# Performance work log

Hardware: AMD Instinct MI355X
Metric: run time of the kernel (lower is better)

## Reference

```python
import jax, jax.numpy as jnp
import numpy as np

B, N, DIM, HEADS = 2, 2048, 1024, 16
DH = DIM // HEADS
SCALE = DH ** -0.5


def setup_inputs() -> dict:
    key = jax.random.key(0)
    k1, k2, k3, k4 = jax.random.split(key, 4)
    x = jax.random.normal(k1, (B, N, DIM), dtype=jnp.float32)
    # nn.Linear weights stored as [out, in]; apply as x @ W.T
    w_qkv = jax.random.normal(k2, (3 * DIM, DIM), dtype=jnp.float32) * (DIM ** -0.5)
    w_out = jax.random.normal(k3, (DIM, DIM), dtype=jnp.float32) * (DIM ** -0.5)
    b_out = jax.random.normal(k4, (DIM,), dtype=jnp.float32) * 0.01
    return {"x": x, "w_qkv": w_qkv, "w_out": w_out, "b_out": b_out}


def reference(x, w_qkv, w_out, b_out):
    b, n, _ = x.shape
    qkv = jnp.einsum('bnd,ed->bne', x, w_qkv)  # [b, n, 3*dim]
    q, k, v = jnp.split(qkv, 3, axis=-1)
    # [b, n, dim] -> [b, heads, n, dim_head]
    def split_heads(t):
        return t.reshape(b, n, HEADS, DH).transpose(0, 2, 1, 3)
    q, k, v = split_heads(q), split_heads(k), split_heads(v)
    attn = jnp.einsum('bhid,bhjd->bhij', q, k) * SCALE  # [b, h, n, n]
    attn = jax.nn.softmax(attn, axis=-1)
    out = jnp.einsum('bhij,bhjd->bhid', attn, v)  # [b, h, n, dh]
    out = out.transpose(0, 2, 1, 3).reshape(b, n, DIM)
    return jnp.einsum('bnd,ed->bne', out, w_out) + b_out
```

## Files before the change

kernel.cpp:

```cpp
#include <hip/hip_runtime.h>
#include <hip/hip_bf16.h>
#include <stdint.h>

#define BB 2
#define NN 2048
#define DIMM 1024
#define HEADS 16
#define DH 64
#define E3 3072
#define LOG2E_ 1.44269504088896f
#define THR_ 8.0f

typedef __bf16 bf16;
typedef __attribute__((ext_vector_type(8))) __bf16 bf16x8;
typedef __attribute__((ext_vector_type(4))) __bf16 bf16x4;
typedef __attribute__((ext_vector_type(4))) float f32x4;

__device__ __forceinline__ void gload_lds16(const void* gsrc, void* ldst) {
  __builtin_amdgcn_global_load_lds(
      (const __attribute__((address_space(1))) uint32_t*)(uintptr_t)gsrc,
      (__attribute__((address_space(3))) uint32_t*)(uintptr_t)ldst,
      16, 0, 0);
}

__global__ __launch_bounds__(256)
void convert_all(const float* __restrict__ x, const float* __restrict__ wqkv,
                 const float* __restrict__ wout,
                 bf16* __restrict__ xb, bf16* __restrict__ wqb, bf16* __restrict__ wob) {
  size_t i = (size_t)blockIdx.x * blockDim.x + threadIdx.x;
  const float* src;
  bf16* dst;
  size_t off;
  if (i < 1048576u) { src = x; dst = xb; off = i; }
  else if (i < 1048576u + 786432u) { src = wqkv; dst = wqb; off = i - 1048576u; }
  else { src = wout; dst = wob; off = i - (1048576u + 786432u); }
  float4 v = ((const float4*)src)[off];
  bf16x4 o;
  o[0] = (bf16)v.x; o[1] = (bf16)v.y; o[2] = (bf16)v.z; o[3] = (bf16)v.w;
  *(bf16x4*)(dst + off * 4) = o;
}

#define GDSR(dst, base, off) \
  asm volatile("ds_read_b128 %0, %1 offset:%c2" : "=v"(dst) : "v"(base), "i"(off))

#define GRD12(ABASE, BBASE, OFF) \
  GDSR(af0, ABASE, (OFF));        GDSR(af1, ABASE, (OFF)+2048); \
  GDSR(af2, ABASE, (OFF)+4096);   GDSR(af3, ABASE, (OFF)+6144); \
  GDSR(af4, ABASE, (OFF)+8192);   GDSR(af5, ABASE, (OFF)+10240); \
  GDSR(af6, ABASE, (OFF)+12288);  GDSR(af7, ABASE, (OFF)+14336); \
  GDSR(bf0, BBASE, (OFF));        GDSR(bf1, BBASE, (OFF)+2048); \
  GDSR(bf2, BBASE, (OFF)+4096);   GDSR(bf3, BBASE, (OFF)+6144);

#define GMM32() \
  acc[0][0]=__builtin_amdgcn_mfma_f32_16x16x32_bf16(af0,bf0,acc[0][0],0,0,0); \
  acc[0][1]=__builtin_amdgcn_mfma_f32_16x16x32_bf16(af0,bf1,acc[0][1],0,0,0); \
  acc[0][2]=__builtin_amdgcn_mfma_f32_16x16x32_bf16(af0,bf2,acc[0][2],0,0,0); \
  acc[0][3]=__builtin_amdgcn_mfma_f32_16x16x32_bf16(af0,bf3,acc[0][3],0,0,0); \
  acc[1][0]=__builtin_amdgcn_mfma_f32_16x16x32_bf16(af1,bf0,acc[1][0],0,0,0); \
  acc[1][1]=__builtin_amdgcn_mfma_f32_16x16x32_bf16(af1,bf1,acc[1][1],0,0,0); \
  acc[1][2]=__builtin_amdgcn_mfma_f32_16x16x32_bf16(af1,bf2,acc[1][2],0,0,0); \
  acc[1][3]=__builtin_amdgcn_mfma_f32_16x16x32_bf16(af1,bf3,acc[1][3],0,0,0); \
  acc[2][0]=__builtin_amdgcn_mfma_f32_16x16x32_bf16(af2,bf0,acc[2][0],0,0,0); \
  acc[2][1]=__builtin_amdgcn_mfma_f32_16x16x32_bf16(af2,bf1,acc[2][1],0,0,0); \
  acc[2][2]=__builtin_amdgcn_mfma_f32_16x16x32_bf16(af2,bf2,acc[2][2],0,0,0); \
  acc[2][3]=__builtin_amdgcn_mfma_f32_16x16x32_bf16(af2,bf3,acc[2][3],0,0,0); \
  acc[3][0]=__builtin_amdgcn_mfma_f32_16x16x32_bf16(af3,bf0,acc[3][0],0,0,0); \
  acc[3][1]=__builtin_amdgcn_mfma_f32_16x16x32_bf16(af3,bf1,acc[3][1],0,0,0); \
  acc[3][2]=__builtin_amdgcn_mfma_f32_16x16x32_bf16(af3,bf2,acc[3][2],0,0,0); \
  acc[3][3]=__builtin_amdgcn_mfma_f32_16x16x32_bf16(af3,bf3,acc[3][3],0,0,0); \
  acc[4][0]=__builtin_amdgcn_mfma_f32_16x16x32_bf16(af4,bf0,acc[4][0],0,0,0); \
  acc[4][1]=__builtin_amdgcn_mfma_f32_16x16x32_bf16(af4,bf1,acc[4][1],0,0,0); \
  acc[4][2]=__builtin_amdgcn_mfma_f32_16x16x32_bf16(af4,bf2,acc[4][2],0,0,0); \
  acc[4][3]=__builtin_amdgcn_mfma_f32_16x16x32_bf16(af4,bf3,acc[4][3],0,0,0); \
  acc[5][0]=__builtin_amdgcn_mfma_f32_16x16x32_bf16(af5,bf0,acc[5][0],0,0,0); \
  acc[5][1]=__builtin_amdgcn_mfma_f32_16x16x32_bf16(af5,bf1,acc[5][1],0,0,0); \
  acc[5][2]=__builtin_amdgcn_mfma_f32_16x16x32_bf16(af5,bf2,acc[5][2],0,0,0); \
  acc[5][3]=__builtin_amdgcn_mfma_f32_16x16x32_bf16(af5,bf3,acc[5][3],0,0,0); \
  acc[6][0]=__builtin_amdgcn_mfma_f32_16x16x32_bf16(af6,bf0,acc[6][0],0,0,0); \
  acc[6][1]=__builtin_amdgcn_mfma_f32_16x16x32_bf16(af6,bf1,acc[6][1],0,0,0); \
  acc[6][2]=__builtin_amdgcn_mfma_f32_16x16x32_bf16(af6,bf2,acc[6][2],0,0,0); \
  acc[6][3]=__builtin_amdgcn_mfma_f32_16x16x32_bf16(af6,bf3,acc[6][3],0,0,0); \
  acc[7][0]=__builtin_amdgcn_mfma_f32_16x16x32_bf16(af7,bf0,acc[7][0],0,0,0); \
  acc[7][1]=__builtin_amdgcn_mfma_f32_16x16x32_bf16(af7,bf1,acc[7][1],0,0,0); \
  acc[7][2]=__builtin_amdgcn_mfma_f32_16x16x32_bf16(af7,bf2,acc[7][2],0,0,0); \
  acc[7][3]=__builtin_amdgcn_mfma_f32_16x16x32_bf16(af7,bf3,acc[7][3],0,0,0);

#define GSTAGE(BUF) { \
  gload_lds16(pA,          smem + (BUF)*32768 + w*1024); \
  gload_lds16(pA + 65536,  smem + (BUF)*32768 + 8192 + w*1024); \
  gload_lds16(pA + 131072, smem + (BUF)*32768 + 16384 + w*1024); \
  gload_lds16(pA + 196608, smem + (BUF)*32768 + 24576 + w*1024); \
  gload_lds16(pB,          smem + 65536 + (BUF)*32768 + w*1024); \
  gload_lds16(pB + 65536,  smem + 65536 + (BUF)*32768 + 8192 + w*1024); \
  gload_lds16(pB + 131072, smem + 65536 + (BUF)*32768 + 16384 + w*1024); \
  gload_lds16(pB + 196608, smem + 65536 + (BUF)*32768 + 24576 + w*1024); \
  pA += 64; pB += 64; }

#define GSTEP(BUF, DOSTAGE) { \
  bf16x8 af0, af1, af2, af3, af4, af5, af6, af7, bf0, bf1, bf2, bf3; \
  GRD12(abase0, bbase0, (BUF)*32768); \
  if (DOSTAGE) { GSTAGE((BUF)^1); } \
  asm volatile("s_waitcnt lgkmcnt(0)" ::: "memory"); \
  __builtin_amdgcn_sched_barrier(0); \
  __builtin_amdgcn_s_setprio(1); \
  GMM32(); \
  __builtin_amdgcn_s_setprio(0); \
  GRD12(abase1, bbase1, (BUF)*32768); \
  asm volatile("s_waitcnt lgkmcnt(0)" ::: "memory"); \
  __builtin_amdgcn_sched_barrier(0); \
  __builtin_amdgcn_s_setprio(1); \
  GMM32(); \
  __builtin_amdgcn_s_setprio(0); \
  if (DOSTAGE) { asm volatile("s_waitcnt vmcnt(0)" ::: "memory"); } \
  __builtin_amdgcn_sched_barrier(0); \
  __builtin_amdgcn_s_barrier(); \
}

__global__ __launch_bounds__(512, 2)
void gemm_qkv(const bf16* __restrict__ A, const bf16* __restrict__ Bw,
              bf16* __restrict__ C) {
  int bid = blockIdx.x;
  bid = (bid & 7) * 24 + (bid >> 3);
  const int nx = bid % 12;
  const int ny = bid / 12;
  const int m0 = ny * 256, n0 = nx * 256;
  const int tid = threadIdx.x;
  const int w = tid >> 6, lane = tid & 63, c = lane & 15, g = lane >> 4;
  const int wr = w >> 2, wc = w & 3;

  __shared__ __align__(16) char smem[131072];
  const uint32_t smem32 = (uint32_t)(uintptr_t)smem;
  const uint32_t abase0 = smem32 + (wr * 128 + c) * 128 + ((g ^ (c & 7)) * 16);
  const uint32_t abase1 = smem32 + (wr * 128 + c) * 128 + (((4 + g) ^ (c & 7)) * 16);
  const uint32_t bbase0 = smem32 + 65536 + (wc * 64 + c) * 128 + ((g ^ (c & 7)) * 16);
  const uint32_t bbase1 = smem32 + 65536 + (wc * 64 + c) * 128 + (((4 + g) ^ (c & 7)) * 16);

  const bf16 *pA, *pB;
  {
    const int r0 = tid >> 3;
    const int cc = (tid & 7) ^ ((tid >> 3) & 7);
    pA = A + (size_t)(m0 + r0) * 1024 + cc * 8;
    pB = Bw + (size_t)(n0 + r0) * 1024 + cc * 8;
  }

  f32x4 acc[8][4] = {};

  GSTAGE(0);
  asm volatile("s_waitcnt vmcnt(0)" ::: "memory");
  __builtin_amdgcn_sched_barrier(0);
  __builtin_amdgcn_s_barrier();

  for (int u = 0; u < 7; ++u) {
    GSTEP(0, 1) GSTEP(1, 1)
  }
  GSTEP(0, 1)
  GSTEP(1, 0)

  const float qsc = (n0 < 1024) ? 0.125f : 1.0f;
#pragma unroll
  for (int fr = 0; fr < 8; ++fr) {
    const int row = m0 + wr * 128 + fr * 16 + g * 4;
#pragma unroll
    for (int fc = 0; fc < 4; ++fc) {
      const int col = n0 + wc * 64 + fc * 16 + c;
#pragma unroll
      for (int r = 0; r < 4; ++r)
        C[(size_t)(row + r) * E3 + col] = (bf16)(acc[fr][fc][r] * qsc);
    }
  }
}

#define ORD8(ABASE, BBASE, OFF) \
  GDSR(ao0, ABASE, (OFF));        GDSR(ao1, ABASE, (OFF)+2048); \
  GDSR(ao2, ABASE, (OFF)+4096);   GDSR(ao3, ABASE, (OFF)+6144); \
  GDSR(bo0, BBASE, (OFF));        GDSR(bo1, BBASE, (OFF)+2048); \
  GDSR(bo2, BBASE, (OFF)+4096);   GDSR(bo3, BBASE, (OFF)+6144);

#define OMM16() \
  acc[0][0]=__builtin_amdgcn_mfma_f32_16x16x32_bf16(ao0,bo0,acc[0][0],0,0,0); \
  acc[0][1]=__builtin_amdgcn_mfma_f32_16x16x32_bf16(ao0,bo1,acc[0][1],0,0,0); \
  acc[0][2]=__builtin_amdgcn_mfma_f32_16x16x32_bf16(ao0,bo2,acc[0][2],0,0,0); \
  acc[0][3]=__builtin_amdgcn_mfma_f32_16x16x32_bf16(ao0,bo3,acc[0][3],0,0,0); \
  acc[1][0]=__builtin_amdgcn_mfma_f32_16x16x32_bf16(ao1,bo0,acc[1][0],0,0,0); \
  acc[1][1]=__builtin_amdgcn_mfma_f32_16x16x32_bf16(ao1,bo1,acc[1][1],0,0,0); \
  acc[1][2]=__builtin_amdgcn_mfma_f32_16x16x32_bf16(ao1,bo2,acc[1][2],0,0,0); \
  acc[1][3]=__builtin_amdgcn_mfma_f32_16x16x32_bf16(ao1,bo3,acc[1][3],0,0,0); \
  acc[2][0]=__builtin_amdgcn_mfma_f32_16x16x32_bf16(ao2,bo0,acc[2][0],0,0,0); \
  acc[2][1]=__builtin_amdgcn_mfma_f32_16x16x32_bf16(ao2,bo1,acc[2][1],0,0,0); \
  acc[2][2]=__builtin_amdgcn_mfma_f32_16x16x32_bf16(ao2,bo2,acc[2][2],0,0,0); \
  acc[2][3]=__builtin_amdgcn_mfma_f32_16x16x32_bf16(ao2,bo3,acc[2][3],0,0,0); \
  acc[3][0]=__builtin_amdgcn_mfma_f32_16x16x32_bf16(ao3,bo0,acc[3][0],0,0,0); \
  acc[3][1]=__builtin_amdgcn_mfma_f32_16x16x32_bf16(ao3,bo1,acc[3][1],0,0,0); \
  acc[3][2]=__builtin_amdgcn_mfma_f32_16x16x32_bf16(ao3,bo2,acc[3][2],0,0,0); \
  acc[3][3]=__builtin_amdgcn_mfma_f32_16x16x32_bf16(ao3,bo3,acc[3][3],0,0,0);

#define OSTAGE(BUF) { \
  gload_lds16(pA,          smem + (BUF)*16384 + w*1024); \
  gload_lds16(pA + 32768,  smem + (BUF)*16384 + 4096 + w*1024); \
  gload_lds16(pA + 65536,  smem + (BUF)*16384 + 8192 + w*1024); \
  gload_lds16(pA + 98304,  smem + (BUF)*16384 + 12288 + w*1024); \
  gload_lds16(pB,          smem + 32768 + (BUF)*16384 + w*1024); \
  gload_lds16(pB + 32768,  smem + 32768 + (BUF)*16384 + 4096 + w*1024); \
  gload_lds16(pB + 65536,  smem + 32768 + (BUF)*16384 + 8192 + w*1024); \
  gload_lds16(pB + 98304,  smem + 32768 + (BUF)*16384 + 12288 + w*1024); \
  pA += 64; pB += 64; }

#define OSTEP(BUF, DOSTAGE) { \
  bf16x8 ao0, ao1, ao2, ao3, bo0, bo1, bo2, bo3; \
  ORD8(abase0, bbase0, (BUF)*16384); \
  if (DOSTAGE) { OSTAGE((BUF)^1); } \
  asm volatile("s_waitcnt lgkmcnt(0)" ::: "memory"); \
  __builtin_amdgcn_sched_barrier(0); \
  __builtin_amdgcn_s_setprio(1); \
  OMM16(); \
  __builtin_amdgcn_s_setprio(0); \
  ORD8(abase1, bbase1, (BUF)*16384); \
  asm volatile("s_waitcnt lgkmcnt(0)" ::: "memory"); \
  __builtin_amdgcn_sched_barrier(0); \
  __builtin_amdgcn_s_setprio(1); \
  OMM16(); \
  __builtin_amdgcn_s_setprio(0); \
  if (DOSTAGE) { asm volatile("s_waitcnt vmcnt(0)" ::: "memory"); } \
  __builtin_amdgcn_sched_barrier(0); \
  __builtin_amdgcn_s_barrier(); \
}

__global__ __launch_bounds__(256, 2)
void gemm_out(const bf16* __restrict__ A, const bf16* __restrict__ Bw,
              float* __restrict__ C, const float* __restrict__ bias) {
  int bid = blockIdx.x;
  bid = (bid & 7) * 32 + (bid >> 3);
  const int nx = bid & 7;
  const int ny = bid >> 3;
  const int m0 = ny * 128, n0 = nx * 128;
  const int tid = threadIdx.x;
  const int w = tid >> 6, lane = tid & 63, c = lane & 15, g = lane >> 4;
  const int wr = w >> 1, wc = w & 1;

  __shared__ __align__(16) char smem[65536];
  const uint32_t smem32 = (uint32_t)(uintptr_t)smem;
  const uint32_t abase0 = smem32 + (wr * 64 + c) * 128 + ((g ^ (c & 7)) * 16);
  const uint32_t abase1 = smem32 + (wr * 64 + c) * 128 + (((4 + g) ^ (c & 7)) * 16);
  const uint32_t bbase0 = smem32 + 32768 + (wc * 64 + c) * 128 + ((g ^ (c & 7)) * 16);
  const uint32_t bbase1 = smem32 + 32768 + (wc * 64 + c) * 128 + (((4 + g) ^ (c & 7)) * 16);

  const bf16 *pA, *pB;
  {
    const int r0 = tid >> 3;
    const int cc = (tid & 7) ^ ((tid >> 3) & 7);
    pA = A + (size_t)(m0 + r0) * 1024 + cc * 8;
    pB = Bw + (size_t)(n0 + r0) * 1024 + cc * 8;
  }

  f32x4 acc[4][4] = {};

  OSTAGE(0);
  asm volatile("s_waitcnt vmcnt(0)" ::: "memory");
  __builtin_amdgcn_sched_barrier(0);
  __builtin_amdgcn_s_barrier();

  for (int u = 0; u < 7; ++u) {
    OSTEP(0, 1) OSTEP(1, 1)
  }
  OSTEP(0, 1)
  OSTEP(1, 0)

#pragma unroll
  for (int i = 0; i < 4; ++i) {
    const int row = m0 + wr * 64 + i * 16 + g * 4;
#pragma unroll
    for (int j = 0; j < 4; ++j) {
      const int col = n0 + wc * 64 + j * 16 + c;
      const float bv = bias[col];
#pragma unroll
      for (int r = 0; r < 4; ++r)
        C[(size_t)(row + r) * DIMM + col] = acc[i][j][r] + bv;
    }
  }
}

#define DSR128(dst, base, off) \
  asm volatile("ds_read_b128 %0, %1 offset:%c2" : "=v"(dst) : "v"(base), "i"(off))
#define DSTR(dst, base, off) \
  asm volatile("ds_read_b64_tr_b16 %0, %1 offset:%c2" : "=v"(dst) : "v"(base), "i"(off))

#define KF_ALL(KB) \
  DSR128(kf[0][0], kb0, (KB)*8192 + 0);    DSR128(kf[0][1], kb1, (KB)*8192 + 0); \
  DSR128(kf[1][0], kb0, (KB)*8192 + 2048); DSR128(kf[1][1], kb1, (KB)*8192 + 2048); \
  DSR128(kf[2][0], kb0, (KB)*8192 + 4096); DSR128(kf[2][1], kb1, (KB)*8192 + 4096); \
  DSR128(kf[3][0], kb0, (KB)*8192 + 6144); DSR128(kf[3][1], kb1, (KB)*8192 + 6144);

#define TRPAIR(f, ks, VP) \
  DSTR(tlo[f][ks], tb, (VP)*8192 + (f)*2048 + (ks)*1024); \
  DSTR(thi[f][ks], tb, (VP)*8192 + (f)*2048 + (ks)*1024 + 512);
#define TR_ALL(VP) \
  TRPAIR(0,0,VP) TRPAIR(0,1,VP) TRPAIR(1,0,VP) TRPAIR(1,1,VP) \
  TRPAIR(2,0,VP) TRPAIR(2,1,VP) TRPAIR(3,0,VP) TRPAIR(3,1,VP)

#define SMAX_A(SPRV, qc) { \
  f32x4 vm = SPRV[0][qc]; \
  _Pragma("unroll") for (int j = 1; j < 4; ++j) \
    _Pragma("unroll") for (int r = 0; r < 4; ++r) vm[r] = fmaxf(vm[r], SPRV[j][qc][r]); \
  float rmax = fmaxf(fmaxf(vm[0], vm[1]), fmaxf(vm[2], vm[3])); \
  rmax = fmaxf(rmax, __shfl_xor(rmax, 16, 64)); \
  rmax = fmaxf(rmax, __shfl_xor(rmax, 32, 64)); \
  const float rmax2 = rmax * LOG2E_; \
  if (!__all(rmax2 <= mrun[qc] + THR_)) { \
    const float mnew = fmaxf(mrun[qc], rmax2); \
    const float fac = __builtin_amdgcn_exp2f(mrun[qc] - mnew); \
    mrun[qc] = mnew; \
    _Pragma("unroll") for (int f = 0; f < 4; ++f) oacc[f][qc] *= fac; \
    lacc[qc] *= fac; \
  } }

#define SMAX_B(SPRV, qc) { \
  const float negm = -mrun[qc]; \
  f32x4 p[4]; \
  _Pragma("unroll") for (int j = 0; j < 4; ++j) \
    _Pragma("unroll") for (int r = 0; r < 4; ++r) \
      p[j][r] = __builtin_amdgcn_exp2f(fmaf(SPRV[j][qc][r], LOG2E_, negm)); \
  _Pragma("unroll") for (int ks = 0; ks < 2; ++ks) \
    _Pragma("unroll") for (int r = 0; r < 4; ++r) { \
      vb[qc][ks][r] = (bf16)p[ks][r]; vb[qc][ks][4 + r] = (bf16)p[ks + 2][r]; \
    } }

#define QK_ALL(SCUR) \
  _Pragma("unroll") for (int j = 0; j < 4; ++j) { \
    f32x4 z = {0.f, 0.f, 0.f, 0.f}; \
    f32x4 s0 = __builtin_amdgcn_mfma_f32_16x16x32_bf16(kf[j][0], qf[0][0], z, 0, 0, 0); \
    s0 = __builtin_amdgcn_mfma_f32_16x16x32_bf16(kf[j][1], qf[0][1], s0, 0, 0, 0); \
    SCUR[j][0] = s0; \
    f32x4 s1 = __builtin_amdgcn_mfma_f32_16x16x32_bf16(kf[j][0], qf[1][0], z, 0, 0, 0); \
    s1 = __builtin_amdgcn_mfma_f32_16x16x32_bf16(kf[j][1], qf[1][1], s1, 0, 0, 0); \
    SCUR[j][1] = s1; }

#define PV_ALL() \
  _Pragma("unroll") for (int f = 0; f < 4; ++f) \
    _Pragma("unroll") for (int ks = 0; ks < 2; ++ks) { \
      bf16x8 va; \
      _Pragma("unroll") for (int e = 0; e < 4; ++e) { va[e] = tlo[f][ks][e]; va[4+e] = thi[f][ks][e]; } \
      oacc[f][0] = __builtin_amdgcn_mfma_f32_16x16x32_bf16(va, vb[0][ks], oacc[f][0], 0, 0, 0); \
      oacc[f][1] = __builtin_amdgcn_mfma_f32_16x16x32_bf16(va, vb[1][ks], oacc[f][1], 0, 0, 0); \
    } \
  lacc[0] = __builtin_amdgcn_mfma_f32_16x16x32_bf16(ones, vb[0][0], lacc[0], 0, 0, 0); \
  lacc[0] = __builtin_amdgcn_mfma_f32_16x16x32_bf16(ones, vb[0][1], lacc[0], 0, 0, 0); \
  lacc[1] = __builtin_amdgcn_mfma_f32_16x16x32_bf16(ones, vb[1][0], lacc[1], 0, 0, 0); \
  lacc[1] = __builtin_amdgcn_mfma_f32_16x16x32_bf16(ones, vb[1][1], lacc[1], 0, 0, 0);

#define STEP(KB, VN, VP, SCUR, SPRV, DOSTAGE, DOPREV) { \
  if (DOSTAGE) { \
    gload_lds16(pK0, smem + ((KB)^1)*8192 + w*1024); \
    gload_lds16(pK1, smem + ((KB)^1)*8192 + 4096 + w*1024); \
    gload_lds16(pV0, smem + 16384 + (VN)*8192 + w*1024); \
    gload_lds16(pV1, smem + 16384 + (VN)*8192 + 4096 + w*1024); \
    pK0 += 64*E3; pK1 += 64*E3; pV0 += 64*E3; pV1 += 64*E3; \
  } \
  if (DOPREV) { SMAX_A(SPRV, 0); SMAX_A(SPRV, 1); } \
  __builtin_amdgcn_sched_barrier(0); \
  KF_ALL(KB); \
  if (DOPREV) { TR_ALL(VP); } \
  if (DOPREV) { SMAX_B(SPRV, 0); SMAX_B(SPRV, 1); } \
  if (DOPREV) { asm volatile("s_waitcnt lgkmcnt(15)" ::: "memory"); } \
  else        { asm volatile("s_waitcnt lgkmcnt(0)" ::: "memory"); } \
  __builtin_amdgcn_sched_barrier(0); \
  __builtin_amdgcn_s_setprio(1); \
  QK_ALL(SCUR); \
  __builtin_amdgcn_s_setprio(0); \
  if (DOPREV) { \
    asm volatile("s_waitcnt lgkmcnt(0)" ::: "memory"); \
    __builtin_amdgcn_sched_barrier(0); \
    __builtin_amdgcn_s_setprio(1); \
    PV_ALL(); \
    __builtin_amdgcn_s_setprio(0); \
  } \
  __syncthreads(); \
}

__global__ __launch_bounds__(256, 2)
void flash_attn(const bf16* __restrict__ qkv, bf16* __restrict__ attb) {
  int bid = blockIdx.x;
  bid = (bid & 7) * 64 + (bid >> 3);
  const int tid = threadIdx.x;
  const int w = tid >> 6;
  const int lane = tid & 63;
  const int c = lane & 15;
  const int g = lane >> 4;
  const int qt = bid & 15;
  const int bh = bid >> 4;
  const int b = bh >> 4;
  const int h = bh & 15;
  const int q0 = qt * 128 + w * 32;

  __shared__ __align__(16) char smem[49152];
  const uint32_t smem32 = (uint32_t)(uintptr_t)smem;

  const uint32_t kb0 = smem32 + c * 128 + ((g ^ (c & 7)) * 16);
  const uint32_t kb1 = smem32 + c * 128 + (((4 + g) ^ (c & 7)) * 16);
  const uint32_t tb  = smem32 + 16384 + lane * 8;

  bf16x8 qf[2][2];
#pragma unroll
  for (int qc = 0; qc < 2; ++qc) {
    const size_t qbase = (size_t)(b * NN + q0 + qc * 16 + c) * E3 + h * 64;
    qf[qc][0] = *(const bf16x8*)(qkv + qbase + g * 8);
    qf[qc][1] = *(const bf16x8*)(qkv + qbase + 32 + g * 8);
  }

  bf16x8 ones;
#pragma unroll
  for (int e = 0; e < 8; ++e) ones[e] = (bf16)1.0f;

  const bf16 *pK0, *pK1, *pV0, *pV1;
  {
    int tK0 = tid, tK1 = 256 + tid;
    int r0 = tK0 >> 3, s0 = (tK0 & 7) ^ (r0 & 7);
    int r1 = tK1 >> 3, s1 = (tK1 & 7) ^ (r1 & 7);
    pK0 = qkv + (size_t)(b * NN + r0) * E3 + 1024 + h * 64 + s0 * 8;
    pK1 = qkv + (size_t)(b * NN + r1) * E3 + 1024 + h * 64 + s1 * 8;
    int sv0 = tid, sv1 = 256 + tid;
    int f0 = sv0 >> 7, ks0 = (sv0 >> 6) & 1, o0 = (sv0 >> 5) & 1,
        g0 = (sv0 >> 3) & 3, j0 = (sv0 >> 1) & 3, i0 = sv0 & 1;
    int f1 = sv1 >> 7, ks1 = (sv1 >> 6) & 1, o1 = (sv1 >> 5) & 1,
        g1 = (sv1 >> 3) & 3, j1 = (sv1 >> 1) & 3, i1 = sv1 & 1;
    int key0 = 32 * o0 + 16 * ks0 + 4 * g0 + j0;
    int key1 = 32 * o1 + 16 * ks1 + 4 * g1 + j1;
    pV0 = qkv + (size_t)(b * NN + key0) * E3 + 2048 + h * 64 + f0 * 16 + i0 * 8;
    pV1 = qkv + (size_t)(b * NN + key1) * E3 + 2048 + h * 64 + f1 * 16 + i1 * 8;
  }

  f32x4 oacc[4][2] = {};
  f32x4 lacc[2] = {};
  float mrun[2] = {-1e30f, -1e30f};
  f32x4 sA[4][2], sB[4][2];
  bf16x8 kf[4][2];
  bf16x4 tlo[4][2], thi[4][2];
  bf16x8 vb[2][2];

  gload_lds16(pK0, smem + w * 1024);
  gload_lds16(pK1, smem + 4096 + w * 1024);
  gload_lds16(pV0, smem + 16384 + w * 1024);
  gload_lds16(pV1, smem + 16384 + 4096 + w * 1024);
  pK0 += 64 * E3; pK1 += 64 * E3; pV0 += 64 * E3; pV1 += 64 * E3;
  __syncthreads();

  STEP(0, 1, 0, sA, sB, 1, 0)
  for (int to = 1; to <= 25; to += 4) {
    STEP(1, 2, 0, sB, sA, 1, 1)
    STEP(0, 3, 1, sA, sB, 1, 1)
    STEP(1, 0, 2, sB, sA, 1, 1)
    STEP(0, 1, 3, sA, sB, 1, 1)
  }
  STEP(1, 2, 0, sB, sA, 1, 1)
  STEP(0, 3, 1, sA, sB, 1, 1)
  STEP(1, 0, 2, sB, sA, 0, 1)

  SMAX_A(sB, 0); SMAX_A(sB, 1);
  TR_ALL(3);
  SMAX_B(sB, 0); SMAX_B(sB, 1);
  asm volatile("s_waitcnt lgkmcnt(0)" ::: "memory");
  __builtin_amdgcn_sched_barrier(0);
  PV_ALL();

#pragma unroll
  for (int qc = 0; qc < 2; ++qc) {
    const float inv = __builtin_amdgcn_rcpf(lacc[qc][0]);
    const size_t row = (size_t)(b * NN + q0 + qc * 16 + c);
#pragma unroll
    for (int f = 0; f < 4; ++f) {
      bf16x4 o;
#pragma unroll
      for (int r = 0; r < 4; ++r) o[r] = (bf16)(oacc[f][qc][r] * inv);
      *(bf16x4*)(attb + row * 1024 + h * 64 + f * 16 + 4 * g) = o;
    }
  }
}

extern "C" void kernel_launch(void* const* d_in, const int* in_sizes, int n_in,
                              void* d_out, int out_size, void* d_ws, size_t ws_size,
                              hipStream_t stream) {
  const float* x = (const float*)d_in[0];
  const float* wqkv = (const float*)d_in[1];
  const float* wout = (const float*)d_in[2];
  const float* bout = (const float*)d_in[3];

  char* ws = (char*)d_ws;
  bf16* xb   = (bf16*)(ws);
  bf16* wqb  = (bf16*)(ws + 8388608);
  bf16* wob  = (bf16*)(ws + 14680064);
  bf16* qkvb = (bf16*)(ws + 16777216);
  bf16* attb = (bf16*)(ws + 41943040);

  convert_all<<<8192, 256, 0, stream>>>(x, wqkv, wout, xb, wqb, wob);
  gemm_qkv<<<192, 512, 0, stream>>>(xb, wqb, qkvb);
  flash_attn<<<512, 256, 0, stream>>>(qkvb, attb);
  gemm_out<<<256, 256, 0, stream>>>(attb, wob, (float*)d_out, bout);
}
```

Before: 106.6 us.

## Restructure flash attention into single-wave blocks with single-buffered K/V staging

Each flash attention block now holds one 64-thread wave that covers 32 queries, and 2048 blocks are launched. Previously four waves shared a double-buffered K/V tile in 48KB of LDS and synchronised across the block. Each wave now loads its own 64-key K/V tile into 16KB of LDS with no block barrier, and the cross-step software pipeline of QK and softmax is dropped. This trades away K/V reuse across four waves, so global/L2 traffic for K/V rises fourfold, and it serialises load and compute within a step. In return there are no __syncthreads, LDS use is smaller, and more blocks can be resident.

Measured after the change: 125.4 us. 17.6% more time.

```diff
diff --git a/kernel.cpp b/kernel.cpp
--- a/kernel.cpp
+++ b/kernel.cpp
@@ -279,28 +279,28 @@
   }
 }
 
-#define DSR128(dst, base, off) \
+#define FDSR(dst, base, off) \
   asm volatile("ds_read_b128 %0, %1 offset:%c2" : "=v"(dst) : "v"(base), "i"(off))
-#define DSTR(dst, base, off) \
+#define FDSTR(dst, base, off) \
   asm volatile("ds_read_b64_tr_b16 %0, %1 offset:%c2" : "=v"(dst) : "v"(base), "i"(off))
 
-#define KF_ALL(KB) \
-  DSR128(kf[0][0], kb0, (KB)*8192 + 0);    DSR128(kf[0][1], kb1, (KB)*8192 + 0); \
-  DSR128(kf[1][0], kb0, (KB)*8192 + 2048); DSR128(kf[1][1], kb1, (KB)*8192 + 2048); \
-  DSR128(kf[2][0], kb0, (KB)*8192 + 4096); DSR128(kf[2][1], kb1, (KB)*8192 + 4096); \
-  DSR128(kf[3][0], kb0, (KB)*8192 + 6144); DSR128(kf[3][1], kb1, (KB)*8192 + 6144);
-
-#define TRPAIR(f, ks, VP) \
-  DSTR(tlo[f][ks], tb, (VP)*8192 + (f)*2048 + (ks)*1024); \
-  DSTR(thi[f][ks], tb, (VP)*8192 + (f)*2048 + (ks)*1024 + 512);
-#define TR_ALL(VP) \
-  TRPAIR(0,0,VP) TRPAIR(0,1,VP) TRPAIR(1,0,VP) TRPAIR(1,1,VP) \
-  TRPAIR(2,0,VP) TRPAIR(2,1,VP) TRPAIR(3,0,VP) TRPAIR(3,1,VP)
-
-#define SMAX_A(SPRV, qc) { \
-  f32x4 vm = SPRV[0][qc]; \
+#define FKF_ALL() \
+  FDSR(kf[0][0], kb0, 0);    FDSR(kf[0][1], kb1, 0); \
+  FDSR(kf[1][0], kb0, 2048); FDSR(kf[1][1], kb1, 2048); \
+  FDSR(kf[2][0], kb0, 4096); FDSR(kf[2][1], kb1, 4096); \
+  FDSR(kf[3][0], kb0, 6144); FDSR(kf[3][1], kb1, 6144);
+
+#define FTRPAIR(f, ks) \
+  FDSTR(tlo[f][ks], tb, (f)*2048 + (ks)*1024); \
+  FDSTR(thi[f][ks], tb, (f)*2048 + (ks)*1024 + 512);
+#define FTR_ALL() \
+  FTRPAIR(0,0) FTRPAIR(0,1) FTRPAIR(1,0) FTRPAIR(1,1) \
+  FTRPAIR(2,0) FTRPAIR(2,1) FTRPAIR(3,0) FTRPAIR(3,1)
+
+#define FSMAX_A(qc) { \
+  f32x4 vm = sacc[0][qc]; \
   _Pragma("unroll") for (int j = 1; j < 4; ++j) \
-    _Pragma("unroll") for (int r = 0; r < 4; ++r) vm[r] = fmaxf(vm[r], SPRV[j][qc][r]); \
+    _Pragma("unroll") for (int r = 0; r < 4; ++r) vm[r] = fmaxf(vm[r], sacc[j][qc][r]); \
   float rmax = fmaxf(fmaxf(vm[0], vm[1]), fmaxf(vm[2], vm[3])); \
   rmax = fmaxf(rmax, __shfl_xor(rmax, 16, 64)); \
   rmax = fmaxf(rmax, __shfl_xor(rmax, 32, 64)); \
@@ -313,28 +313,28 @@
     lacc[qc] *= fac; \
   } }
 
-#define SMAX_B(SPRV, qc) { \
+#define FSMAX_B(qc) { \
   const float negm = -mrun[qc]; \
   f32x4 p[4]; \
   _Pragma("unroll") for (int j = 0; j < 4; ++j) \
     _Pragma("unroll") for (int r = 0; r < 4; ++r) \
-      p[j][r] = __builtin_amdgcn_exp2f(fmaf(SPRV[j][qc][r], LOG2E_, negm)); \
+      p[j][r] = __builtin_amdgcn_exp2f(fmaf(sacc[j][qc][r], LOG2E_, negm)); \
   _Pragma("unroll") for (int ks = 0; ks < 2; ++ks) \
     _Pragma("unroll") for (int r = 0; r < 4; ++r) { \
       vb[qc][ks][r] = (bf16)p[ks][r]; vb[qc][ks][4 + r] = (bf16)p[ks + 2][r]; \
     } }
 
-#define QK_ALL(SCUR) \
+#define FQK_ALL() \
   _Pragma("unroll") for (int j = 0; j < 4; ++j) { \
     f32x4 z = {0.f, 0.f, 0.f, 0.f}; \
     f32x4 s0 = __builtin_amdgcn_mfma_f32_16x16x32_bf16(kf[j][0], qf[0][0], z, 0, 0, 0); \
     s0 = __builtin_amdgcn_mfma_f32_16x16x32_bf16(kf[j][1], qf[0][1], s0, 0, 0, 0); \
-    SCUR[j][0] = s0; \
+    sacc[j][0] = s0; \
     f32x4 s1 = __builtin_amdgcn_mfma_f32_16x16x32_bf16(kf[j][0], qf[1][0], z, 0, 0, 0); \
     s1 = __builtin_amdgcn_mfma_f32_16x16x32_bf16(kf[j][1], qf[1][1], s1, 0, 0, 0); \
-    SCUR[j][1] = s1; }
-
-#define PV_ALL() \
+    sacc[j][1] = s1; }
+
+#define FPV_ALL() \
   _Pragma("unroll") for (int f = 0; f < 4; ++f) \
     _Pragma("unroll") for (int ks = 0; ks < 2; ++ks) { \
       bf16x8 va; \
@@ -347,56 +347,44 @@
   lacc[1] = __builtin_amdgcn_mfma_f32_16x16x32_bf16(ones, vb[1][0], lacc[1], 0, 0, 0); \
   lacc[1] = __builtin_amdgcn_mfma_f32_16x16x32_bf16(ones, vb[1][1], lacc[1], 0, 0, 0);
 
-#define STEP(KB, VN, VP, SCUR, SPRV, DOSTAGE, DOPREV) { \
-  if (DOSTAGE) { \
-    gload_lds16(pK0, smem + ((KB)^1)*8192 + w*1024); \
-    gload_lds16(pK1, smem + ((KB)^1)*8192 + 4096 + w*1024); \
-    gload_lds16(pV0, smem + 16384 + (VN)*8192 + w*1024); \
-    gload_lds16(pV1, smem + 16384 + (VN)*8192 + 4096 + w*1024); \
-    pK0 += 64*E3; pK1 += 64*E3; pV0 += 64*E3; pV1 += 64*E3; \
-  } \
-  if (DOPREV) { SMAX_A(SPRV, 0); SMAX_A(SPRV, 1); } \
-  __builtin_amdgcn_sched_barrier(0); \
-  KF_ALL(KB); \
-  if (DOPREV) { TR_ALL(VP); } \
-  if (DOPREV) { SMAX_B(SPRV, 0); SMAX_B(SPRV, 1); } \
-  if (DOPREV) { asm volatile("s_waitcnt lgkmcnt(15)" ::: "memory"); } \
-  else        { asm volatile("s_waitcnt lgkmcnt(0)" ::: "memory"); } \
-  __builtin_amdgcn_sched_barrier(0); \
-  __builtin_amdgcn_s_setprio(1); \
-  QK_ALL(SCUR); \
-  __builtin_amdgcn_s_setprio(0); \
-  if (DOPREV) { \
-    asm volatile("s_waitcnt lgkmcnt(0)" ::: "memory"); \
-    __builtin_amdgcn_sched_barrier(0); \
-    __builtin_amdgcn_s_setprio(1); \
-    PV_ALL(); \
-    __builtin_amdgcn_s_setprio(0); \
-  } \
-  __syncthreads(); \
-}
-
-__global__ __launch_bounds__(256, 2)
+#define FSTAGE() { \
+  gload_lds16(pK + 0*8*E3, smem + 0*1024); \
+  gload_lds16(pK + 1*8*E3, smem + 1*1024); \
+  gload_lds16(pK + 2*8*E3, smem + 2*1024); \
+  gload_lds16(pK + 3*8*E3, smem + 3*1024); \
+  gload_lds16(pK + 4*8*E3, smem + 4*1024); \
+  gload_lds16(pK + 5*8*E3, smem + 5*1024); \
+  gload_lds16(pK + 6*8*E3, smem + 6*1024); \
+  gload_lds16(pK + 7*8*E3, smem + 7*1024); \
+  gload_lds16(pV0 + 0*16, smem + 8192 + 0*1024); \
+  gload_lds16(pV1 + 0*16, smem + 8192 + 1*1024); \
+  gload_lds16(pV0 + 1*16, smem + 8192 + 2*1024); \
+  gload_lds16(pV1 + 1*16, smem + 8192 + 3*1024); \
+  gload_lds16(pV0 + 2*16, smem + 8192 + 4*1024); \
+  gload_lds16(pV1 + 2*16, smem + 8192 + 5*1024); \
+  gload_lds16(pV0 + 3*16, smem + 8192 + 6*1024); \
+  gload_lds16(pV1 + 3*16, smem + 8192 + 7*1024); \
+  pK += 64*E3; pV0 += 64*E3; pV1 += 64*E3; }
+
+__global__ __launch_bounds__(64, 2)
 void flash_attn(const bf16* __restrict__ qkv, bf16* __restrict__ attb) {
   int bid = blockIdx.x;
-  bid = (bid & 7) * 64 + (bid >> 3);
-  const int tid = threadIdx.x;
-  const int w = tid >> 6;
-  const int lane = tid & 63;
+  bid = (bid & 7) * 256 + (bid >> 3);
+  const int lane = threadIdx.x;
   const int c = lane & 15;
   const int g = lane >> 4;
-  const int qt = bid & 15;
-  const int bh = bid >> 4;
+  const int qt = bid & 63;
+  const int bh = bid >> 6;
   const int b = bh >> 4;
   const int h = bh & 15;
-  const int q0 = qt * 128 + w * 32;
-
-  __shared__ __align__(16) char smem[49152];
+  const int q0 = qt * 32;
+
+  __shared__ __align__(16) char smem[16384];
   const uint32_t smem32 = (uint32_t)(uintptr_t)smem;
 
   const uint32_t kb0 = smem32 + c * 128 + ((g ^ (c & 7)) * 16);
   const uint32_t kb1 = smem32 + c * 128 + (((4 + g) ^ (c & 7)) * 16);
-  const uint32_t tb  = smem32 + 16384 + lane * 8;
+  const uint32_t tb  = smem32 + 8192 + lane * 8;
 
   bf16x8 qf[2][2];
 #pragma unroll
@@ -410,56 +398,52 @@
 #pragma unroll
   for (int e = 0; e < 8; ++e) ones[e] = (bf16)1.0f;
 
-  const bf16 *pK0, *pK1, *pV0, *pV1;
+  const bf16 *pK, *pV0, *pV1;
   {
-    int tK0 = tid, tK1 = 256 + tid;
-    int r0 = tK0 >> 3, s0 = (tK0 & 7) ^ (r0 & 7);
-    int r1 = tK1 >> 3, s1 = (tK1 & 7) ^ (r1 & 7);
-    pK0 = qkv + (size_t)(b * NN + r0) * E3 + 1024 + h * 64 + s0 * 8;
-    pK1 = qkv + (size_t)(b * NN + r1) * E3 + 1024 + h * 64 + s1 * 8;
-    int sv0 = tid, sv1 = 256 + tid;
-    int f0 = sv0 >> 7, ks0 = (sv0 >> 6) & 1, o0 = (sv0 >> 5) & 1,
-        g0 = (sv0 >> 3) & 3, j0 = (sv0 >> 1) & 3, i0 = sv0 & 1;
-    int f1 = sv1 >> 7, ks1 = (sv1 >> 6) & 1, o1 = (sv1 >> 5) & 1,
-        g1 = (sv1 >> 3) & 3, j1 = (sv1 >> 1) & 3, i1 = sv1 & 1;
-    int key0 = 32 * o0 + 16 * ks0 + 4 * g0 + j0;
-    int key1 = 32 * o1 + 16 * ks1 + 4 * g1 + j1;
-    pV0 = qkv + (size_t)(b * NN + key0) * E3 + 2048 + h * 64 + f0 * 16 + i0 * 8;
-    pV1 = qkv + (size_t)(b * NN + key1) * E3 + 2048 + h * 64 + f1 * 16 + i1 * 8;
+    pK = qkv + (size_t)(b * NN + (lane >> 3)) * E3 + 1024 + h * 64
+             + (((lane & 7) ^ ((lane >> 3) & 7)) * 8);
+    const int oct = lane >> 5, gg = (lane >> 3) & 3, j = (lane >> 1) & 3,
+              i1 = lane & 1;
+    const int key0 = 32 * oct + 4 * gg + j;
+    pV0 = qkv + (size_t)(b * NN + key0) * E3 + 2048 + h * 64 + i1 * 8;
+    pV1 = pV0 + 16 * E3;
   }
 
   f32x4 oacc[4][2] = {};
   f32x4 lacc[2] = {};
   float mrun[2] = {-1e30f, -1e30f};
-  f32x4 sA[4][2], sB[4][2];
+  f32x4 sacc[4][2];
   bf16x8 kf[4][2];
   bf16x4 tlo[4][2], thi[4][2];
   bf16x8 vb[2][2];
 
-  gload_lds16(pK0, smem + w * 1024);
-  gload_lds16(pK1, smem + 4096 + w * 1024);
-  gload_lds16(pV0, smem + 16384 + w * 1024);
-  gload_lds16(pV1, smem + 16384 + 4096 + w * 1024);
-  pK0 += 64 * E3; pK1 += 64 * E3; pV0 += 64 * E3; pV1 += 64 * E3;
-  __syncthreads();
-
-  STEP(0, 1, 0, sA, sB, 1, 0)
-  for (int to = 1; to <= 25; to += 4) {
-    STEP(1, 2, 0, sB, sA, 1, 1)
-    STEP(0, 3, 1, sA, sB, 1, 1)
-    STEP(1, 0, 2, sB, sA, 1, 1)
-    STEP(0, 1, 3, sA, sB, 1, 1)
-  }
-  STEP(1, 2, 0, sB, sA, 1, 1)
-  STEP(0, 3, 1, sA, sB, 1, 1)
-  STEP(1, 0, 2, sB, sA, 0, 1)
-
-  SMAX_A(sB, 0); SMAX_A(sB, 1);
-  TR_ALL(3);
-  SMAX_B(sB, 0); SMAX_B(sB, 1);
-  asm volatile("s_waitcnt lgkmcnt(0)" ::: "memory");
-  __builtin_amdgcn_sched_barrier(0);
-  PV_ALL();
+  FSTAGE();
+
+  for (int t = 0; t < 32; ++t) {
+    asm volatile("s_waitcnt vmcnt(8)" ::: "memory");
+    __builtin_amdgcn_sched_barrier(0);
+    FKF_ALL();
+    asm volatile("s_waitcnt lgkmcnt(0)" ::: "memory");
+    __builtin_amdgcn_sched_barrier(0);
+    __builtin_amdgcn_s_setprio(1);
+    FQK_ALL();
+    __builtin_amdgcn_s_setprio(0);
+
+    FSMAX_A(0); FSMAX_A(1);
+
+    asm volatile("s_waitcnt vmcnt(0)" ::: "memory");
+    __builtin_amdgcn_sched_barrier(0);
+    FTR_ALL();
+    FSMAX_B(0); FSMAX_B(1);
+    asm volatile("s_waitcnt lgkmcnt(0)" ::: "memory");
+    __builtin_amdgcn_sched_barrier(0);
+
+    if (t < 31) { FSTAGE(); }
+
+    __builtin_amdgcn_s_setprio(1);
+    FPV_ALL();
+    __builtin_amdgcn_s_setprio(0);
+  }
 
 #pragma unroll
   for (int qc = 0; qc < 2; ++qc) {
@@ -492,6 +476,6 @@
 
   convert_all<<<8192, 256, 0, stream>>>(x, wqkv, wout, xb, wqb, wob);
   gemm_qkv<<<192, 512, 0, stream>>>(xb, wqb, qkvb);
-  flash_attn<<<512, 256, 0, stream>>>(qkvb, attb);
+  flash_attn<<<2048, 64, 0, stream>>>(qkvb, attb);
   gemm_out<<<256, 256, 0, stream>>>(attb, wob, (float*)d_out, bout);
 }
```
